# Kernel optimization log

Measured on AMD Instinct MI355X. Metric: run time of the kernel, lower is better.

The kernel has to match this reference:

```python
import jax, jax.numpy as jnp
import numpy as np

NUM_HEADS = 8
KEY_DIM = 16
D = 32          # attn_ratio * key_dim
DH = D * NUM_HEADS  # 256
NH_KD = KEY_DIM * NUM_HEADS  # 128
DIM = 256


def _conv1x1_bn(x, W, s, b):
    # 1x1 conv (no bias) followed by eval-mode BatchNorm folded to affine.
    # x: [B, Cin, H, W], W: [Cout, Cin], s/b: [Cout]
    y = jnp.einsum('oc,bchw->bohw', W, x)
    return y * s[None, :, None, None] + b[None, :, None, None]


def setup_inputs() -> dict:
    key = jax.random.key(0)
    ks = jax.random.split(key, 16)
    B, C, H, Wd = 2, DIM, 64, 64
    rgb = jax.random.normal(ks[0], (B, C, H, Wd), dtype=jnp.float32)
    edge = jax.random.normal(ks[1], (B, C, H, Wd), dtype=jnp.float32)

    def conv_w(k, o, i):
        return jax.random.normal(k, (o, i), dtype=jnp.float32) * (1.0 / np.sqrt(i))

    def bn(k, c):
        k1, k2 = jax.random.split(k)
        s = jax.random.uniform(k1, (c,), dtype=jnp.float32, minval=0.5, maxval=1.5)
        b = jax.random.normal(k2, (c,), dtype=jnp.float32) * 0.1
        return s, b

    Wq = conv_w(ks[2], NH_KD, C); sq, bq = bn(ks[3], NH_KD)
    Wk = conv_w(ks[4], NH_KD, C); sk, bk = bn(ks[5], NH_KD)
    Wv = conv_w(ks[6], DH, C);   sv, bv = bn(ks[7], DH)
    Wp = conv_w(ks[8], C, DH);   sp, bp = bn(ks[9], C)
    return dict(rgb=rgb, edge=edge, Wq=Wq, sq=sq, bq=bq, Wk=Wk, sk=sk, bk=bk,
                Wv=Wv, sv=sv, bv=bv, Wp=Wp, sp=sp, bp=bp)


def reference(rgb, edge, Wq, sq, bq, Wk, sk, bk, Wv, sv, bv, Wp, sp, bp):
    B, C, H, Wd = rgb.shape
    N = H * Wd
    # Q from rgb, K/V from edge (all 1x1 conv + BN)
    qq = _conv1x1_bn(rgb, Wq, sq, bq).reshape(B, NUM_HEADS, KEY_DIM, N)
    qq = jnp.transpose(qq, (0, 1, 3, 2))                       # [B,h,N,kd]
    kk = _conv1x1_bn(edge, Wk, sk, bk).reshape(B, NUM_HEADS, KEY_DIM, N)  # [B,h,kd,N]
    vv = _conv1x1_bn(edge, Wv, sv, bv).reshape(B, NUM_HEADS, D, N)
    vv = jnp.transpose(vv, (0, 1, 3, 2))                       # [B,h,N,d]
    # NOTE: original forward does NOT apply self.scale -- faithful omission.
    attn = jnp.einsum('bhnk,bhkm->bhnm', qq, kk)               # [B,h,N,N]
    attn = jax.nn.softmax(attn, axis=-1)
    xx = jnp.einsum('bhnm,bhmd->bhnd', attn, vv)               # [B,h,N,d]
    xx = jnp.transpose(xx, (0, 1, 3, 2)).reshape(B, DH, H, Wd)
    xx = jax.nn.relu(xx)                                       # activation before proj conv
    xx = _conv1x1_bn(xx, Wp, sp, bp)                           # [B,C,H,W]
    return xx
```

## Files before the change

### kernel.cpp

```cpp
#include <hip/hip_runtime.h>
#include <hip/hip_bf16.h>

#define NB 2
#define CIN 256
#define NPIX 4096
#define NHEADS 8
#define KD 16
#define DV 32
#define DH 256
#define NHKD 128

typedef short bf16x8 __attribute__((ext_vector_type(8)));
typedef short s16x4 __attribute__((ext_vector_type(4)));
typedef float f32x4 __attribute__((ext_vector_type(4)));
typedef float f32x16 __attribute__((ext_vector_type(16)));
typedef unsigned int u32x2 __attribute__((ext_vector_type(2)));
typedef unsigned int u32x4 __attribute__((ext_vector_type(4)));

#define LOG2E 1.4426950408889634f

static __device__ __forceinline__ unsigned short f2bf(float f) {
    __hip_bfloat16 h = __float2bfloat16(f);
    return __builtin_bit_cast(unsigned short, h);
}

__global__ __launch_bounds__(256) void k_prep(
    const float* __restrict__ Wq, const float* __restrict__ Wk,
    const float* __restrict__ Wv, const float* __restrict__ Wp,
    unsigned short* __restrict__ wq, unsigned short* __restrict__ wk,
    unsigned short* __restrict__ wv, unsigned short* __restrict__ wp)
{
    int i = blockIdx.x * 256 + threadIdx.x;
    if (i < NHKD * CIN) { wq[i] = f2bf(Wq[i]); wk[i] = f2bf(Wk[i]); }
    if (i < DH * CIN)   { wv[i] = f2bf(Wv[i]); wp[i] = f2bf(Wp[i]); }
}

__global__ __launch_bounds__(256) void k_qkv(
    const float* __restrict__ rgb, const float* __restrict__ edge,
    const unsigned short* __restrict__ wq, const unsigned short* __restrict__ wk,
    const unsigned short* __restrict__ wv,
    const float* __restrict__ sq, const float* __restrict__ bq,
    const float* __restrict__ sk, const float* __restrict__ bk,
    const float* __restrict__ sv, const float* __restrict__ bv,
    unsigned short* __restrict__ Qw, unsigned short* __restrict__ Kw,
    unsigned short* __restrict__ Vw)
{
    const int nb = blockIdx.x;
    const int ob = blockIdx.y;
    const int b  = blockIdx.z;
    const int tid = threadIdx.x;
    const int wave = tid >> 6, lane = tid & 63;
    const int cl = lane & 15, g = lane >> 4;

    const float* X; const unsigned short* W; const float* sc; const float* bi;
    int obase, job;
    if (ob < 2)      { X = rgb  + (size_t)b*CIN*NPIX; W = wq; sc = sq; bi = bq; obase = ob*64;     job = 0; }
    else if (ob < 4) { X = edge + (size_t)b*CIN*NPIX; W = wk; sc = sk; bi = bk; obase = (ob-2)*64; job = 1; }
    else             { X = edge + (size_t)b*CIN*NPIX; W = wv; sc = sv; bi = bv; obase = (ob-4)*64; job = 2; }

    __shared__ float xt[32 * 65];

    f32x4 acc[4];
    #pragma unroll
    for (int i = 0; i < 4; i++) acc[i] = (f32x4)0.f;

    const int n0 = nb * 64;
    const int ow = obase + wave * 16 + cl;
    const unsigned short* Wrow = W + (size_t)ow * CIN;

    for (int kt = 0; kt < 8; kt++) {
        __syncthreads();
        {
            int tr = tid >> 6;
            int tc = tid & 63;
            #pragma unroll
            for (int r = 0; r < 8; r++) {
                int c_local = r * 4 + tr;
                xt[c_local * 65 + tc] = X[(size_t)(kt * 32 + c_local) * NPIX + n0 + tc];
            }
        }
        __syncthreads();
        #pragma unroll
        for (int ns = 0; ns < 4; ns++) {
            bf16x8 a;
            #pragma unroll
            for (int j = 0; j < 8; j++)
                a[j] = (short)f2bf(xt[(8 * g + j) * 65 + ns * 16 + cl]);
            bf16x8 wfrag = *reinterpret_cast<const bf16x8*>(Wrow + kt * 32 + 8 * g);
            acc[ns] = __builtin_amdgcn_mfma_f32_16x16x32_bf16(a, wfrag, acc[ns], 0, 0, 0);
        }
    }

    const float sco = sc[ow], bio = bi[ow];
    if (job == 2) {
        int h = ow >> 5, d = ow & 31;
        unsigned short* dst = Vw + ((size_t)((b * 8 + h) * 32 + d)) * NPIX;
        #pragma unroll
        for (int ns = 0; ns < 4; ns++) {
            int nr = n0 + ns * 16 + 4 * g;
            s16x4 pk;
            #pragma unroll
            for (int r = 0; r < 4; r++) pk[r] = (short)f2bf(acc[ns][r] * sco + bio);
            *reinterpret_cast<s16x4*>(dst + nr) = pk;
        }
    } else {
        float scq = sco, biq = bio;
        if (job == 0) { scq *= LOG2E; biq *= LOG2E; }
        unsigned short* base = (job == 0) ? Qw : Kw;
        int h = ow >> 4, kd = ow & 15;
        unsigned short* dst = base + ((size_t)(b * 8 + h) * NPIX) * KD + kd;
        #pragma unroll
        for (int ns = 0; ns < 4; ns++)
            #pragma unroll
            for (int r = 0; r < 4; r++) {
                int nr = n0 + ns * 16 + 4 * g + r;
                dst[(size_t)nr * KD] = f2bf(acc[ns][r] * scq + biq);
            }
    }
}

typedef const unsigned int __attribute__((address_space(1)))* gp_t;
typedef unsigned int __attribute__((address_space(3)))* lp_t;

__global__ __launch_bounds__(256) void k_attn(
    const unsigned short* __restrict__ Qw, const unsigned short* __restrict__ Kw,
    const unsigned short* __restrict__ Vw, unsigned short* __restrict__ Ow)
{
    const int qg = blockIdx.x;
    const int bh = blockIdx.y;
    const int tid = threadIdx.x;
    const int wave = tid >> 6, lane = tid & 63;
    const int l31 = lane & 31, hi = lane >> 5;

    __shared__ union {
        unsigned short v[4][2048];
        float o[4][32][32];
    } sh;
    __shared__ float shl[4][32];

    const unsigned short* Kbase = Kw + (size_t)bh * NPIX * KD;
    const unsigned short* Vbase = Vw + (size_t)bh * DV * NPIX;

    const int q0 = qg * 32;
    const bf16x8 qf = *(const bf16x8*)(Qw + ((size_t)bh * NPIX + q0 + l31) * KD + 8 * hi);

    const unsigned short* Kln = Kbase + (size_t)l31 * KD + 8 * hi;
#define KF0(T) (*(const bf16x8*)(Kln + ((T) * 64 + 0) * KD))
#define KF1(T) (*(const bf16x8*)(Kln + ((T) * 64 + 32) * KD))

    const int scb = ((lane & 7) * 16) ^ ((lane >> 3) << 4);
    const unsigned short* Vln = Vbase + (size_t)(lane >> 3) * NPIX + (scb >> 1);

    const int vsw = (l31 & 7) << 4;

    f32x16 o = (f32x16)0.f;
    float l_run = 0.f;
    const f32x16 z16 = (f32x16)0.f;

    for (int t = 0; t < 16; ++t) {
        const int T = wave * 16 + t;
        bf16x8 ka0 = KF0(T);
        bf16x8 ka1 = KF1(T);
        #pragma unroll
        for (int j = 0; j < 4; ++j)
            __builtin_amdgcn_global_load_lds(
                (gp_t)(const void*)(Vln + (size_t)j * 8 * NPIX + T * 64),
                (lp_t)(void*)(&sh.v[wave][j * 512]), 16, 0, 0);

        f32x16 s0 = __builtin_amdgcn_mfma_f32_32x32x16_bf16(ka0, qf, z16, 0, 0, 0);
        f32x16 s1 = __builtin_amdgcn_mfma_f32_32x32x16_bf16(ka1, qf, z16, 0, 0, 0);
        #pragma unroll
        for (int i = 0; i < 16; ++i) s0[i] = __builtin_amdgcn_exp2f(s0[i]);
        #pragma unroll
        for (int i = 0; i < 16; ++i) s1[i] = __builtin_amdgcn_exp2f(s1[i]);

        float t16[16];
        #pragma unroll
        for (int i = 0; i < 16; ++i) t16[i] = s0[i] + s1[i];
        #pragma unroll
        for (int i = 0; i < 8; ++i) t16[i] += t16[i + 8];
        #pragma unroll
        for (int i = 0; i < 4; ++i) t16[i] += t16[i + 4];
        t16[0] += t16[2]; t16[1] += t16[3];
        l_run += t16[0] + t16[1];

        unsigned up[16];
        #pragma unroll
        for (int ss = 0; ss < 8; ++ss) {
            up[ss]     = (unsigned)f2bf(s0[2*ss]) | ((unsigned)f2bf(s0[2*ss+1]) << 16);
            up[8 + ss] = (unsigned)f2bf(s1[2*ss]) | ((unsigned)f2bf(s1[2*ss+1]) << 16);
        }
        #pragma unroll
        for (int gg = 0; gg < 4; ++gg) {
            u32x2 r0 = __builtin_amdgcn_permlane32_swap(up[4*gg+0], up[4*gg+2], false, false);
            up[4*gg+0] = r0.x; up[4*gg+2] = r0.y;
            u32x2 r1 = __builtin_amdgcn_permlane32_swap(up[4*gg+1], up[4*gg+3], false, false);
            up[4*gg+1] = r1.x; up[4*gg+3] = r1.y;
        }

        asm volatile("s_waitcnt vmcnt(0)" ::: "memory");
        #pragma unroll
        for (int c = 0; c < 4; ++c) {
            u32x4 av;
            av.x = up[4*c + 0];
            av.y = up[4*c + 1];
            av.z = up[4*c + 2];
            av.w = up[4*c + 3];
            const int vidx = wave * 2048 + ((l31 * 128 + ((32 * c + 16 * hi) ^ vsw)) >> 1);
            bf16x8 vb = *(const bf16x8*)(&sh.v[0][vidx]);
            o = __builtin_amdgcn_mfma_f32_32x32x16_bf16(
                    __builtin_bit_cast(bf16x8, av), vb, o, 0, 0, 0);
        }
    }
#undef KF0
#undef KF1

    l_run += __shfl_xor(l_run, 32, 64);

    #pragma unroll
    for (int r = 0; r < 16; ++r) {
        const int qr = (r & 3) + 8 * (r >> 2) + 4 * hi;
        sh.o[wave][qr][l31] = o[r];
    }
    if (hi == 0) shl[wave][l31] = l_run;
    __syncthreads();

    const int q = tid >> 3;
    const int d0 = (tid & 7) * 4;
    const float lsum = shl[0][q] + shl[1][q] + shl[2][q] + shl[3][q];
    const float linv = __builtin_amdgcn_rcpf(lsum);
    float v[4];
    #pragma unroll
    for (int i = 0; i < 4; ++i) {
        float s = sh.o[0][q][d0+i] + sh.o[1][q][d0+i] + sh.o[2][q][d0+i] + sh.o[3][q][d0+i];
        v[i] = fmaxf(s * linv, 0.f);
    }
    const int b = bh >> 3, h = bh & 7;
    u32x2 pk;
    pk.x = (unsigned)f2bf(v[0]) | ((unsigned)f2bf(v[1]) << 16);
    pk.y = (unsigned)f2bf(v[2]) | ((unsigned)f2bf(v[3]) << 16);
    *reinterpret_cast<u32x2*>(Ow + ((size_t)b * NPIX + q0 + q) * DH + h * DV + d0) = pk;
}

__global__ __launch_bounds__(256) void k_proj(
    const unsigned short* __restrict__ Xo, const unsigned short* __restrict__ wp,
    const float* __restrict__ sp, const float* __restrict__ bp,
    float* __restrict__ out)
{
    const int nb = blockIdx.x;
    const int b  = blockIdx.y;
    const int tid = threadIdx.x;
    const int wave = tid >> 6, lane = tid & 63;
    const int cl = lane & 15, g = lane >> 4;

    const int cbase = wave * 64;
    f32x4 acc[4][4];
    #pragma unroll
    for (int i = 0; i < 4; i++)
        #pragma unroll
        for (int j = 0; j < 4; j++) acc[i][j] = (f32x4)0.f;

    const unsigned short* Xb = Xo + ((size_t)b * NPIX + nb * 64) * DH;

    #pragma unroll
    for (int kt = 0; kt < 8; kt++) {
        bf16x8 afr[4];
        #pragma unroll
        for (int cs = 0; cs < 4; cs++)
            afr[cs] = *reinterpret_cast<const bf16x8*>(wp + (size_t)(cbase + cs * 16 + cl) * DH + kt * 32 + 8 * g);
        #pragma unroll
        for (int ns = 0; ns < 4; ns++) {
            bf16x8 bfr = *reinterpret_cast<const bf16x8*>(Xb + (size_t)(ns * 16 + cl) * DH + kt * 32 + 8 * g);
            #pragma unroll
            for (int cs = 0; cs < 4; cs++)
                acc[cs][ns] = __builtin_amdgcn_mfma_f32_16x16x32_bf16(afr[cs], bfr, acc[cs][ns], 0, 0, 0);
        }
    }

    #pragma unroll
    for (int cs = 0; cs < 4; cs++)
        #pragma unroll
        for (int r = 0; r < 4; r++) {
            int c = cbase + cs * 16 + 4 * g + r;
            float scv = sp[c], biv = bp[c];
            float* dst = out + ((size_t)b * DH + c) * NPIX + nb * 64;
            #pragma unroll
            for (int ns = 0; ns < 4; ns++)
                dst[ns * 16 + cl] = acc[cs][ns][r] * scv + biv;
        }
}

extern "C" void kernel_launch(void* const* d_in, const int* in_sizes, int n_in,
                              void* d_out, int out_size, void* d_ws, size_t ws_size,
                              hipStream_t stream) {
    const float* rgb  = (const float*)d_in[0];
    const float* edge = (const float*)d_in[1];
    const float* Wq = (const float*)d_in[2];
    const float* sq = (const float*)d_in[3];
    const float* bq = (const float*)d_in[4];
    const float* Wk = (const float*)d_in[5];
    const float* sk = (const float*)d_in[6];
    const float* bk = (const float*)d_in[7];
    const float* Wv = (const float*)d_in[8];
    const float* sv = (const float*)d_in[9];
    const float* bv = (const float*)d_in[10];
    const float* Wp = (const float*)d_in[11];
    const float* sp = (const float*)d_in[12];
    const float* bp = (const float*)d_in[13];
    float* out = (float*)d_out;

    char* ws = (char*)d_ws;
    unsigned short* wq = (unsigned short*)(ws + 0);
    unsigned short* wk = (unsigned short*)(ws + (64 << 10));
    unsigned short* wv = (unsigned short*)(ws + (128 << 10));
    unsigned short* wp = (unsigned short*)(ws + (256 << 10));
    size_t o = 384 << 10;
    unsigned short* Qw = (unsigned short*)(ws + o); o += (size_t)16 * NPIX * KD * 2;
    unsigned short* Kw = (unsigned short*)(ws + o); o += (size_t)16 * NPIX * KD * 2;
    unsigned short* Vw = (unsigned short*)(ws + o); o += (size_t)16 * DV * NPIX * 2;
    unsigned short* Ow = (unsigned short*)(ws + o);

    k_prep<<<dim3(256), dim3(256), 0, stream>>>(Wq, Wk, Wv, Wp, wq, wk, wv, wp);
    k_qkv<<<dim3(64, 8, NB), dim3(256), 0, stream>>>(rgb, edge, wq, wk, wv,
                                                     sq, bq, sk, bk, sv, bv, Qw, Kw, Vw);
    k_attn<<<dim3(128, 16), dim3(256), 0, stream>>>(Qw, Kw, Vw, Ow);
    k_proj<<<dim3(64, NB), dim3(256), 0, stream>>>(Ow, wp, sp, bp, out);
}
```

Before: 95.67 us.

## Double-buffer V tiles and prefetch K fragments one iteration ahead in attention

Each wave's V staging area in LDS is split into two buffers. The K fragments and V tile for the next key block are issued one iteration early, and the loop is fully unrolled. The row-sum reduction is rewritten with packed float2 adds, and a barrier is added before the output reuses the shared union. The goal is to hide global-load latency behind the MFMA and exp work. However, the vmcnt(0) wait still blocks on the freshly issued prefetch, so the overlap gained may be limited, and LDS use doubles.

```diff
diff --git a/kernel.cpp b/kernel.cpp
--- a/kernel.cpp
+++ b/kernel.cpp
@@ -12,6 +12,7 @@
 
 typedef short bf16x8 __attribute__((ext_vector_type(8)));
 typedef short s16x4 __attribute__((ext_vector_type(4)));
+typedef float f32x2 __attribute__((ext_vector_type(2)));
 typedef float f32x4 __attribute__((ext_vector_type(4)));
 typedef float f32x16 __attribute__((ext_vector_type(16)));
 typedef unsigned int u32x2 __attribute__((ext_vector_type(2)));
@@ -133,10 +134,9 @@
     const int l31 = lane & 31, hi = lane >> 5;
 
     __shared__ union {
-        unsigned short v[4][2048];
-        float o[4][32][32];
+        unsigned short v[4][2][2048];
+        struct { float o[4][32][32]; float l[4][32]; } c;
     } sh;
-    __shared__ float shl[4][32];
 
     const unsigned short* Kbase = Kw + (size_t)bh * NPIX * KD;
     const unsigned short* Vbase = Vw + (size_t)bh * DV * NPIX;
@@ -150,6 +150,10 @@
 
     const int scb = ((lane & 7) * 16) ^ ((lane >> 3) << 4);
     const unsigned short* Vln = Vbase + (size_t)(lane >> 3) * NPIX + (scb >> 1);
+#define STAGE(T, BUF) do { _Pragma("unroll") for (int j = 0; j < 4; ++j) \
+    __builtin_amdgcn_global_load_lds( \
+        (gp_t)(const void*)(Vln + (size_t)j * 8 * NPIX + (size_t)(T) * 64), \
+        (lp_t)(void*)(&sh.v[wave][BUF][j * 512]), 16, 0, 0); } while (0)
 
     const int vsw = (l31 & 7) << 4;
 
@@ -157,15 +161,20 @@
     float l_run = 0.f;
     const f32x16 z16 = (f32x16)0.f;
 
+    const int T0 = wave * 16;
+    bf16x8 ka0 = KF0(T0), ka1 = KF1(T0);
+    bf16x8 kb0, kb1;
+    STAGE(T0, 0);
+
+    #pragma unroll
     for (int t = 0; t < 16; ++t) {
-        const int T = wave * 16 + t;
-        bf16x8 ka0 = KF0(T);
-        bf16x8 ka1 = KF1(T);
-        #pragma unroll
-        for (int j = 0; j < 4; ++j)
-            __builtin_amdgcn_global_load_lds(
-                (gp_t)(const void*)(Vln + (size_t)j * 8 * NPIX + T * 64),
-                (lp_t)(void*)(&sh.v[wave][j * 512]), 16, 0, 0);
+        const int T = T0 + t;
+        const int cur = t & 1;
+        if (t < 15) {
+            kb0 = KF0(T + 1);
+            kb1 = KF1(T + 1);
+            STAGE(T + 1, cur ^ 1);
+        }
 
         f32x16 s0 = __builtin_amdgcn_mfma_f32_32x32x16_bf16(ka0, qf, z16, 0, 0, 0);
         f32x16 s1 = __builtin_amdgcn_mfma_f32_32x32x16_bf16(ka1, qf, z16, 0, 0, 0);
@@ -174,15 +183,17 @@
         #pragma unroll
         for (int i = 0; i < 16; ++i) s1[i] = __builtin_amdgcn_exp2f(s1[i]);
 
-        float t16[16];
-        #pragma unroll
-        for (int i = 0; i < 16; ++i) t16[i] = s0[i] + s1[i];
-        #pragma unroll
-        for (int i = 0; i < 8; ++i) t16[i] += t16[i + 8];
-        #pragma unroll
-        for (int i = 0; i < 4; ++i) t16[i] += t16[i + 4];
-        t16[0] += t16[2]; t16[1] += t16[3];
-        l_run += t16[0] + t16[1];
+        f32x2 r[8];
+        #pragma unroll
+        for (int i = 0; i < 8; ++i) {
+            f32x2 a = {s0[2*i], s0[2*i+1]};
+            f32x2 b = {s1[2*i], s1[2*i+1]};
+            r[i] = a + b;
+        }
+        r[0] += r[4]; r[1] += r[5]; r[2] += r[6]; r[3] += r[7];
+        r[0] += r[2]; r[1] += r[3];
+        r[0] += r[1];
+        l_run += r[0].x + r[0].y;
 
         unsigned up[16];
         #pragma unroll
@@ -199,6 +210,7 @@
         }
 
         asm volatile("s_waitcnt vmcnt(0)" ::: "memory");
+
         #pragma unroll
         for (int c = 0; c < 4; ++c) {
             u32x4 av;
@@ -206,33 +218,36 @@
             av.y = up[4*c + 1];
             av.z = up[4*c + 2];
             av.w = up[4*c + 3];
-            const int vidx = wave * 2048 + ((l31 * 128 + ((32 * c + 16 * hi) ^ vsw)) >> 1);
-            bf16x8 vb = *(const bf16x8*)(&sh.v[0][vidx]);
+            const int vidx = (l31 * 128 + ((32 * c + 16 * hi) ^ vsw)) >> 1;
+            bf16x8 vb = *(const bf16x8*)(&sh.v[wave][cur][vidx]);
             o = __builtin_amdgcn_mfma_f32_32x32x16_bf16(
                     __builtin_bit_cast(bf16x8, av), vb, o, 0, 0, 0);
         }
+        ka0 = kb0; ka1 = kb1;
     }
 #undef KF0
 #undef KF1
+#undef STAGE
 
     l_run += __shfl_xor(l_run, 32, 64);
 
+    __syncthreads();
     #pragma unroll
     for (int r = 0; r < 16; ++r) {
         const int qr = (r & 3) + 8 * (r >> 2) + 4 * hi;
-        sh.o[wave][qr][l31] = o[r];
-    }
-    if (hi == 0) shl[wave][l31] = l_run;
+        sh.c.o[wave][qr][l31] = o[r];
+    }
+    if (hi == 0) sh.c.l[wave][l31] = l_run;
     __syncthreads();
 
     const int q = tid >> 3;
     const int d0 = (tid & 7) * 4;
-    const float lsum = shl[0][q] + shl[1][q] + shl[2][q] + shl[3][q];
+    const float lsum = sh.c.l[0][q] + sh.c.l[1][q] + sh.c.l[2][q] + sh.c.l[3][q];
     const float linv = __builtin_amdgcn_rcpf(lsum);
     float v[4];
     #pragma unroll
     for (int i = 0; i < 4; ++i) {
-        float s = sh.o[0][q][d0+i] + sh.o[1][q][d0+i] + sh.o[2][q][d0+i] + sh.o[3][q][d0+i];
+        float s = sh.c.o[0][q][d0+i] + sh.c.o[1][q][d0+i] + sh.c.o[2][q][d0+i] + sh.c.o[3][q][d0+i];
         v[i] = fmaxf(s * linv, 0.f);
     }
     const int b = bh >> 3, h = bh & 7;
```

New measurement: 94.99 us. Within noise of the previous version (-0.7%).
